# Performance work log

Measured on AMD Instinct MI355X. Metric: run time of the kernel, lower is better.

## Reference

```python
import jax, jax.numpy as jnp
import numpy as np

B, N, F_IN = 16, 2048, 6
NUM_CLASSES = 16


def _laplacian(x):
    # x: [B,N,F]; Gaussian adjacency from pairwise sq distances, then sym-normalized Laplacian
    sq = jnp.sum(x * x, axis=-1, keepdims=True)            # [B,N,1]
    d2 = sq - 2.0 * jnp.einsum('bnf,bmf->bnm', x, x) + jnp.swapaxes(sq, 1, 2)
    adj = jnp.exp(-d2)                                      # [B,N,N]
    dinv = 1.0 / jnp.sqrt(jnp.sum(adj, axis=-1))            # [B,N]
    return jnp.eye(N, dtype=x.dtype) - adj * dinv[:, :, None] * dinv[:, None, :]


def _cheb(x, L, W, b):
    # Chebyshev conv: W [K,Fin,Fout], recursion x_k = 2 L x_{k-1} - x_{k-2}
    K = W.shape[0]
    x0 = x
    out = jnp.einsum('bnf,fg->bng', x0, W[0])
    if K > 1:
        x1 = jnp.einsum('bnm,bmf->bnf', L, x0)
        out = out + jnp.einsum('bnf,fg->bng', x1, W[1])
        for k in range(2, K):
            x2 = 2.0 * jnp.einsum('bnm,bmf->bnf', L, x1) - x0
            out = out + jnp.einsum('bnf,fg->bng', x2, W[k])
            x0, x1 = x1, x2
    return out + b


def setup_inputs() -> dict:
    key = jax.random.key(0)
    ks = jax.random.split(key, 16)

    def w(k, shape, fan_in):
        return jax.random.normal(k, shape, dtype=jnp.float32) * (1.0 / np.sqrt(fan_in))

    inp = {
        'x': jax.random.normal(ks[0], (B, N, F_IN), dtype=jnp.float32),
        'cat': jax.random.randint(ks[1], (B, 1), 0, NUM_CLASSES),
        'W1': w(ks[2], (6, 22, 128), 22), 'b1': jnp.zeros((128,), jnp.float32),
        'W2': w(ks[3], (5, 128, 512), 128), 'b2': jnp.zeros((512,), jnp.float32),
        'W3': w(ks[4], (3, 512, 1024), 512), 'b3': jnp.zeros((1024,), jnp.float32),
        'fc1_w': w(ks[5], (1024, 512), 1024), 'fc1_b': jnp.zeros((512,), jnp.float32),
        'fc2_w': w(ks[6], (1024, 128), 1024), 'fc2_b': jnp.zeros((128,), jnp.float32),
        'fc3_w': w(ks[7], (128, 50), 128), 'fc3_b': jnp.zeros((50,), jnp.float32),
        'br0': jnp.zeros((1, 1, 128), jnp.float32),
        'br1': jnp.zeros((1, 1, 512), jnp.float32),
        'br2': jnp.zeros((1, 1, 1024), jnp.float32),
        'br3': jnp.zeros((1, 1, 512), jnp.float32),
        'br4': jnp.zeros((1, 1, 128), jnp.float32),
        'br5': jnp.zeros((1, 1, 50), jnp.float32),
    }
    return inp


def reference(x, cat, W1, b1, W2, b2, W3, b3, fc1_w, fc1_b, fc2_w, fc2_b,
              fc3_w, fc3_b, br0, br1, br2, br3, br4, br5):
    L = _laplacian(x)                                        # computed under no_grad in torch
    oh = jax.nn.one_hot(cat[:, 0], NUM_CLASSES, dtype=x.dtype)   # [B,16]
    cat_tiled = jnp.broadcast_to(oh[:, None, :], (x.shape[0], N, NUM_CLASSES))
    h = jnp.concatenate([x, cat_tiled], axis=2)              # [B,N,22]

    h = jax.nn.relu(_cheb(h, L, W1, b1) + br0)               # [B,N,128]
    h = jax.nn.relu(_cheb(h, L, W2, b2) + br1)               # [B,N,512]
    x1 = h
    h = jax.nn.relu(_cheb(h, L, W3, b3) + br2)               # [B,N,1024]

    h = jax.nn.relu(h @ fc1_w + fc1_b + br3)                 # [B,N,512]
    h = jnp.concatenate([h, x1], axis=2)                     # [B,N,1024]
    h = jax.nn.relu(h @ fc2_w + fc2_b + br4)                 # [B,N,128]
    h = jax.nn.relu(h @ fc3_w + fc3_b + br5)                 # [B,N,50]
    return h
```

## Files before the change

### kernel.cpp

```cpp
#include <hip/hip_runtime.h>

#define BB 16
#define NN 2048
#define FIN 6
#define MTOT (BB*NN)

typedef unsigned short u16;
typedef __attribute__((ext_vector_type(8))) short  short8;
typedef __attribute__((ext_vector_type(4))) float  f32x4;

__device__ inline float ldf(const u16* p) {
  unsigned u = ((unsigned)*p) << 16; float f; __builtin_memcpy(&f, &u, 4); return f;
}
__device__ inline u16 tobf(float v) {
  unsigned u; __builtin_memcpy(&u, &v, 4);
  u = (u + 0x7FFFu + ((u >> 16) & 1u)) >> 16;
  return (u16)u;
}
__device__ inline void stf(u16* p, float v) { *p = tobf(v); }

__device__ __forceinline__ void gload16(const u16* g, u16* l) {
  __builtin_amdgcn_global_load_lds(
      (const __attribute__((address_space(1))) void*)g,
      (__attribute__((address_space(3))) void*)l, 16, 0, 0);
}

__global__ __launch_bounds__(256) void k_dpart(const float* __restrict__ x,
                                               float* __restrict__ dsum) {
  __shared__ float xs[512][FIN];
  __shared__ float sqs[512];
  const int b = blockIdx.y;
  const int j0 = blockIdx.z * 512;
  const float* xb = x + (size_t)b * NN * FIN;
  for (int l = threadIdx.x; l < 512 * FIN; l += 256) ((float*)xs)[l] = xb[(size_t)j0 * FIN + l];
  __syncthreads();
  for (int j = threadIdx.x; j < 512; j += 256) {
    float s = 0.f;
#pragma unroll
    for (int f = 0; f < FIN; ++f) { float v = xs[j][f]; s = fmaf(v, v, s); }
    sqs[j] = s;
  }
  __syncthreads();
  const int i = blockIdx.x * 256 + threadIdx.x;
  float xi[FIN];
#pragma unroll
  for (int f = 0; f < FIN; ++f) xi[f] = xb[(size_t)i * FIN + f];
  float sqi = 0.f;
#pragma unroll
  for (int f = 0; f < FIN; ++f) sqi = fmaf(xi[f], xi[f], sqi);
  float a0 = 0.f, a1 = 0.f, a2 = 0.f, a3 = 0.f;
  for (int j = 0; j < 512; j += 4) {
#pragma unroll
    for (int u = 0; u < 4; ++u) {
      const int jj = j + u;
      float dot = 0.f;
#pragma unroll
      for (int f = 0; f < FIN; ++f) dot = fmaf(xs[jj][f], xi[f], dot);
      const float e = __expf(2.f * dot - sqi - sqs[jj]);
      if (u == 0) a0 += e; else if (u == 1) a1 += e; else if (u == 2) a2 += e; else a3 += e;
    }
  }
  atomicAdd(&dsum[b * NN + i], (a0 + a1) + (a2 + a3));
}

__global__ void k_rsq(float* __restrict__ d) {
  const int i = blockIdx.x * 256 + threadIdx.x;
  d[i] = 1.0f / sqrtf(d[i]);
}

__global__ __launch_bounds__(256) void k_lap(const float* __restrict__ x,
                                             const float* __restrict__ dinv,
                                             u16* __restrict__ Lm) {
  const int b = blockIdx.z;
  const int i0 = blockIdx.y * 32;
  const int j0 = blockIdx.x * 256;
  __shared__ float xi[32][FIN];
  __shared__ float di[32];
  const int t = threadIdx.x;
  const float* xb = x + (size_t)b * NN * FIN;
  if (t < 32 * FIN) ((float*)xi)[t] = xb[i0 * FIN + t];
  if (t >= 224) di[t - 224] = dinv[b * NN + i0 + (t - 224)];
  const int j = j0 + t;
  float xj[FIN];
#pragma unroll
  for (int f = 0; f < FIN; ++f) xj[f] = xb[j * FIN + f];
  float sqj = 0.f;
#pragma unroll
  for (int f = 0; f < FIN; ++f) sqj = fmaf(xj[f], xj[f], sqj);
  const float dj = dinv[b * NN + j];
  __syncthreads();
  u16* Lb = Lm + (size_t)b * NN * NN;
#pragma unroll 4
  for (int ii = 0; ii < 32; ++ii) {
    float sqi = 0.f, dot = 0.f;
#pragma unroll
    for (int f = 0; f < FIN; ++f) {
      const float v = xi[ii][f];
      sqi = fmaf(v, v, sqi);
      dot = fmaf(v, xj[f], dot);
    }
    float val = -__expf(2.f * dot - sqi - sqj) * di[ii] * dj;
    if (i0 + ii == j) val += 1.f;
    stf(&Lb[(size_t)(i0 + ii) * NN + j], val);
  }
}

__global__ void k_h0T(const float* __restrict__ x, const int* __restrict__ cat,
                      u16* __restrict__ T1T) {
  const int c = blockIdx.y;
  const int m = blockIdx.x * 256 + threadIdx.x;
  float v;
  if (c < 6) v = x[(size_t)m * 6 + c];
  else v = (cat[m >> 11] == (c - 6)) ? 1.f : 0.f;
  stf(&T1T[(size_t)c * MTOT + m], v);
}

__global__ void k_wt(const float* __restrict__ in, u16* __restrict__ out,
                     int R, int C, int ldo) {
  const int r = blockIdx.x * 256 + threadIdx.x;
  const int c = blockIdx.y;
  if (r < R) stf(&out[(size_t)c * ldo + r], in[(size_t)r * C + c]);
}

__global__ __launch_bounds__(256) void k_actT(const u16* __restrict__ in,
                                              u16* __restrict__ out, int F, int ldo) {
  __shared__ u16 t[64][70];
  const int m0 = blockIdx.x * 64;
  const int f0 = blockIdx.y * 64;
  const int tid = threadIdx.x;
#pragma unroll
  for (int v = 0; v < 4; ++v) {
    const int flat = v * 256 + tid;
    const int fr = flat >> 4;
    const int mq = (flat & 15) * 4;
    ushort4 val = {0, 0, 0, 0};
    if (f0 + fr < F) val = *(const ushort4*)&in[(size_t)(f0 + fr) * MTOT + m0 + mq];
    t[fr][mq + 0] = val.x; t[fr][mq + 1] = val.y;
    t[fr][mq + 2] = val.z; t[fr][mq + 3] = val.w;
  }
  __syncthreads();
#pragma unroll
  for (int v = 0; v < 4; ++v) {
    const int flat = v * 256 + tid;
    const int mr = flat >> 4;
    const int fq = (flat & 15) * 4;
    if (f0 + fq >= F) continue;
    u16* dst = &out[(size_t)(m0 + mr) * ldo + f0 + fq];
    if (f0 + fq + 3 < F) {
      ushort4 o;
      o.x = t[fq + 0][mr]; o.y = t[fq + 1][mr];
      o.z = t[fq + 2][mr]; o.w = t[fq + 3][mr];
      *(ushort4*)dst = o;
    } else {
#pragma unroll
      for (int e = 0; e < 4; ++e)
        if (f0 + fq + e < F) dst[e] = t[fq + e][mr];
    }
  }
}

template <int BM, int BN, int EPI, bool TWOQ, typename OT>
__global__ __launch_bounds__(256) void k_mmL(
    const u16* __restrict__ P, long ldp, int rowsP, long strideP,
    const u16* __restrict__ Q0, long ldq0,
    const u16* __restrict__ Q1, long ldq1, int ksplitT,
    int rowsQ, long strideQ, int K,
    OT* __restrict__ Out, long ldo, long strideO,
    const u16* __restrict__ Prev, float alpha, float beta,
    const float* __restrict__ bias, const float* __restrict__ br, int biasOnI) {
  const int b = blockIdx.z;
  const int i0 = blockIdx.y * BM;
  const int j0 = blockIdx.x * BN;
  const u16* Pb = P + (size_t)b * strideP;
  const u16* Qb0 = Q0 + (size_t)b * strideQ;
  OT* Ob = Out + (size_t)b * strideO;
  const u16* Vb = Prev ? Prev + (size_t)b * strideO : nullptr;

  __shared__ __align__(16) u16 Ps[BM * 64];
  __shared__ __align__(16) u16 Qs[BN * 64];
  const int tid = threadIdx.x;
  const int lane = tid & 63;
  const int w = tid >> 6;
  const int wr = w >> 1, wc = w & 1;
  constexpr int FI = BM / 32;
  constexpr int FJ = BN / 32;
  constexpr int VP = BM / 32;
  constexpr int VQ = BN / 32;
  const int rl = lane >> 3;
  const int kb = (((lane & 7) ^ rl) << 3);

  const u16* prow[VP];
  bool pok[VP];
#pragma unroll
  for (int v = 0; v < VP; ++v) {
    const int c = w + v * 4;
    const int gr = i0 + c * 8 + rl;
    pok[v] = gr < rowsP;
    prow[v] = Pb + (size_t)gr * ldp + kb;
  }
  const u16* qrow[VQ];
  const u16* qrow1[TWOQ ? VQ : 1];
  bool qok[VQ];
#pragma unroll
  for (int v = 0; v < VQ; ++v) {
    const int c = w + v * 4;
    const int gr = j0 + c * 8 + rl;
    qok[v] = gr < rowsQ;
    qrow[v] = Qb0 + (size_t)gr * ldq0 + kb;
    if (TWOQ) qrow1[v] = Q1 + (size_t)b * strideQ + (size_t)gr * ldq1 + kb;
  }

  f32x4 acc[FI][FJ];
#pragma unroll
  for (int i = 0; i < FI; ++i)
#pragma unroll
    for (int j = 0; j < FJ; ++j) acc[i][j] = (f32x4){0.f, 0.f, 0.f, 0.f};

  const int nt = K >> 6;
  for (int t = 0; t < nt; ++t) {
#pragma unroll
    for (int v = 0; v < VP; ++v)
      if (pok[v]) gload16(prow[v] + t * 64, &Ps[(w + v * 4) * 512]);
    if (TWOQ) {
      const bool r1 = (t >= ksplitT);
      const int tq = r1 ? (t - ksplitT) : t;
#pragma unroll
      for (int v = 0; v < VQ; ++v)
        if (qok[v]) gload16((r1 ? qrow1[v] : qrow[v]) + tq * 64, &Qs[(w + v * 4) * 512]);
    } else {
#pragma unroll
      for (int v = 0; v < VQ; ++v)
        if (qok[v]) gload16(qrow[v] + t * 64, &Qs[(w + v * 4) * 512]);
    }
    __syncthreads();
#pragma unroll
    for (int h = 0; h < 2; ++h) {
      short8 pf[FI], qf[FJ];
#pragma unroll
      for (int i = 0; i < FI; ++i) {
        const int r = wr * (BM / 2) + i * 16 + (lane & 15);
        const int c = (h * 32 + ((lane >> 4) * 8)) ^ ((r & 7) << 3);
        pf[i] = *(const short8*)&Ps[r * 64 + c];
      }
#pragma unroll
      for (int j = 0; j < FJ; ++j) {
        const int r = wc * (BN / 2) + j * 16 + (lane & 15);
        const int c = (h * 32 + ((lane >> 4) * 8)) ^ ((r & 7) << 3);
        qf[j] = *(const short8*)&Qs[r * 64 + c];
      }
#pragma unroll
      for (int i = 0; i < FI; ++i)
#pragma unroll
        for (int j = 0; j < FJ; ++j)
          acc[i][j] = __builtin_amdgcn_mfma_f32_16x16x32_bf16(pf[i], qf[j], acc[i][j], 0, 0, 0);
    }
    __syncthreads();
  }

  const int ibase = i0 + wr * (BM / 2);
  const int jbase = j0 + wc * (BN / 2);
#pragma unroll
  for (int j = 0; j < FJ; ++j) {
    const int jj = jbase + j * 16 + (lane & 15);
    if (jj >= rowsQ) continue;
    float bj = 0.f;
    if (EPI == 1 && !biasOnI) bj = bias[jj] + br[jj];
#pragma unroll
    for (int i = 0; i < FI; ++i) {
      const int ii = ibase + i * 16 + ((lane >> 4) << 2);
      f32x4 a = acc[i][j];
      float v[4];
#pragma unroll
      for (int e = 0; e < 4; ++e) {
        float xv = a[e];
        if (EPI == 0) {
          xv *= alpha;
          if (beta != 0.f) xv = fmaf(beta, ldf(&Vb[(size_t)jj * ldo + ii + e]), xv);
        } else {
          float bb = bj;
          if (biasOnI) bb = (ii + e < rowsP) ? (bias[ii + e] + br[ii + e]) : 0.f;
          xv = fmaxf(xv + bb, 0.f);
        }
        v[e] = xv;
      }
      if constexpr (sizeof(OT) == 2) {
        u16* dst = (u16*)&Ob[(size_t)jj * ldo + ii];
        if (ii + 3 < rowsP) {
          ushort4 o; o.x = tobf(v[0]); o.y = tobf(v[1]); o.z = tobf(v[2]); o.w = tobf(v[3]);
          *(ushort4*)dst = o;
        } else {
#pragma unroll
          for (int e = 0; e < 4; ++e) if (ii + e < rowsP) dst[e] = tobf(v[e]);
        }
      } else {
        float* dst = (float*)&Ob[(size_t)jj * ldo + ii];
#pragma unroll
        for (int e = 0; e < 4; ++e) if (ii + e < rowsP) dst[e] = v[e];
      }
    }
  }
}

extern "C" void kernel_launch(void* const* d_in, const int* in_sizes, int n_in,
                              void* d_out, int out_size, void* d_ws, size_t ws_size,
                              hipStream_t stream) {
  const float* x    = (const float*)d_in[0];
  const int*   cat  = (const int*)  d_in[1];
  const float* W1   = (const float*)d_in[2];
  const float* b1   = (const float*)d_in[3];
  const float* W2   = (const float*)d_in[4];
  const float* b2   = (const float*)d_in[5];
  const float* W3   = (const float*)d_in[6];
  const float* b3   = (const float*)d_in[7];
  const float* fc1w = (const float*)d_in[8];
  const float* fc1b = (const float*)d_in[9];
  const float* fc2w = (const float*)d_in[10];
  const float* fc2b = (const float*)d_in[11];
  const float* fc3w = (const float*)d_in[12];
  const float* fc3b = (const float*)d_in[13];
  const float* br0  = (const float*)d_in[14];
  const float* br1  = (const float*)d_in[15];
  const float* br2  = (const float*)d_in[16];
  const float* br3  = (const float*)d_in[17];
  const float* br4  = (const float*)d_in[18];
  const float* br5  = (const float*)d_in[19];

  if (ws_size < 240054784ull) return;

  u16* ws = (u16*)d_ws;
  u16* Wt1p = ws;
  u16* Wt2  = Wt1p + 24576;
  u16* Wt3  = Wt2 + 327680;
  u16* Wtf1 = Wt3 + 1572864;
  u16* Wtf2 = Wtf1 + 524288;
  u16* Wtf3 = Wtf2 + 131072;
  u16* Lbuf = ws + 2586880;
  u16* ACT  = Lbuf + 67108864;

  float* dinv = (float*)ACT;
  u16* T1T   = ACT;
  u16* L1rm  = ACT + 4325376;
  u16* T2T   = ACT;
  u16* L2rm  = ACT + 20971520;
  u16* T3T   = ACT;
  u16* L3rm  = Lbuf;
  u16* h3rm  = ACT;
  u16* fc1o  = ACT + 33554432;
  u16* h5    = ACT;

  const long MT = MTOT;
  const int BIG = 1 << 28;

  hipMemsetAsync(dinv, 0, (size_t)MTOT * 4, stream);
  hipMemsetAsync(Wt1p, 0, 24576 * 2, stream);
  hipMemsetAsync(L1rm, 0, (size_t)MTOT * 192 * 2, stream);

  k_wt<<<dim3(1, 128), 256, 0, stream>>>(W1, Wt1p, 132, 128, 192);
  k_wt<<<dim3(3, 512), 256, 0, stream>>>(W2, Wt2, 640, 512, 640);
  k_wt<<<dim3(6, 1024), 256, 0, stream>>>(W3, Wt3, 1536, 1024, 1536);
  k_wt<<<dim3(4, 512), 256, 0, stream>>>(fc1w, Wtf1, 1024, 512, 1024);
  k_wt<<<dim3(4, 128), 256, 0, stream>>>(fc2w, Wtf2, 1024, 128, 1024);
  k_wt<<<dim3(1, 50), 256, 0, stream>>>(fc3w, Wtf3, 128, 50, 128);

  k_dpart<<<dim3(8, BB, 4), 256, 0, stream>>>(x, dinv);
  k_rsq<<<dim3(MTOT / 256), 256, 0, stream>>>(dinv);
  k_lap<<<dim3(8, 64, BB), 256, 0, stream>>>(x, dinv, Lbuf);

  k_h0T<<<dim3(128, 22), 256, 0, stream>>>(x, cat, T1T);
  {
    const size_t s = (size_t)22 * MT;
    k_mmL<64, 32, 0, false, u16><<<dim3(1, 32, BB), 256, 0, stream>>>(
        Lbuf, NN, NN, (long)NN * NN, T1T, MT, nullptr, 0, BIG, 22, NN,
        NN, T1T + s, MT, NN, nullptr, 1.f, 0.f, nullptr, nullptr, 0);
    for (int k = 2; k < 6; ++k)
      k_mmL<64, 32, 0, false, u16><<<dim3(1, 32, BB), 256, 0, stream>>>(
          Lbuf, NN, NN, (long)NN * NN, T1T + (k - 1) * s, MT, nullptr, 0, BIG, 22, NN,
          NN, T1T + k * s, MT, NN, T1T + (k - 2) * s, 2.f, -1.f, nullptr, nullptr, 0);
  }
  k_actT<<<dim3(512, 3), 256, 0, stream>>>(T1T, L1rm, 132, 192);
  k_mmL<128, 128, 1, false, u16><<<dim3(1, 256, 1), 256, 0, stream>>>(
      L1rm, 192, MTOT, 0, Wt1p, 192, nullptr, 0, BIG, 128, 0,
      192, T2T, MT, 0, nullptr, 0.f, 0.f, b1, br0, 0);

  {
    const size_t s = (size_t)128 * MT;
    k_mmL<64, 128, 0, false, u16><<<dim3(1, 32, BB), 256, 0, stream>>>(
        Lbuf, NN, NN, (long)NN * NN, T2T, MT, nullptr, 0, BIG, 128, NN,
        NN, T2T + s, MT, NN, nullptr, 1.f, 0.f, nullptr, nullptr, 0);
    for (int k = 2; k < 5; ++k)
      k_mmL<64, 128, 0, false, u16><<<dim3(1, 32, BB), 256, 0, stream>>>(
          Lbuf, NN, NN, (long)NN * NN, T2T + (k - 1) * s, MT, nullptr, 0, BIG, 128, NN,
          NN, T2T + k * s, MT, NN, T2T + (k - 2) * s, 2.f, -1.f, nullptr, nullptr, 0);
  }
  k_actT<<<dim3(512, 10), 256, 0, stream>>>(T2T, L2rm, 640, 640);
  k_mmL<128, 128, 1, false, u16><<<dim3(4, 256, 1), 256, 0, stream>>>(
      L2rm, 640, MTOT, 0, Wt2, 640, nullptr, 0, BIG, 512, 0,
      640, T3T, MT, 0, nullptr, 0.f, 0.f, b2, br1, 0);

  {
    const size_t s = (size_t)512 * MT;
    k_mmL<128, 128, 0, false, u16><<<dim3(4, 16, BB), 256, 0, stream>>>(
        Lbuf, NN, NN, (long)NN * NN, T3T, MT, nullptr, 0, BIG, 512, NN,
        NN, T3T + s, MT, NN, nullptr, 1.f, 0.f, nullptr, nullptr, 0);
    k_mmL<128, 128, 0, false, u16><<<dim3(4, 16, BB), 256, 0, stream>>>(
        Lbuf, NN, NN, (long)NN * NN, T3T + s, MT, nullptr, 0, BIG, 512, NN,
        NN, T3T + 2 * s, MT, NN, T3T, 2.f, -1.f, nullptr, nullptr, 0);
  }
  k_actT<<<dim3(512, 24), 256, 0, stream>>>(T3T, L3rm, 1536, 1536);
  k_mmL<128, 128, 1, false, u16><<<dim3(256, 8, 1), 256, 0, stream>>>(
      Wt3, 1536, 1024, 0, L3rm, 1536, nullptr, 0, BIG, MTOT, 0,
      1536, h3rm, 1024, 0, nullptr, 0.f, 0.f, b3, br2, 1);

  k_mmL<128, 128, 1, false, u16><<<dim3(256, 4, 1), 256, 0, stream>>>(
      Wtf1, 1024, 512, 0, h3rm, 1024, nullptr, 0, BIG, MTOT, 0,
      1024, fc1o, 512, 0, nullptr, 0.f, 0.f, fc1b, br3, 1);
  k_mmL<64, 128, 1, true, u16><<<dim3(256, 2, 1), 256, 0, stream>>>(
      Wtf2, 1024, 128, 0, fc1o, 512, L3rm, 1536, 8, MTOT, 0,
      1024, h5, 128, 0, nullptr, 0.f, 0.f, fc2b, br4, 1);
  k_mmL<64, 128, 1, false, float><<<dim3(256, 1, 1), 256, 0, stream>>>(
      Wtf3, 128, 50, 0, h5, 128, nullptr, 0, BIG, MTOT, 0,
      128, (float*)d_out, 50, 0, nullptr, 0.f, 0.f, fc3b, br5, 1);
}
```

Measured before the change: 1.125 ms.

## Double-buffer LDS tiles in k_mmL to overlap global loads with MFMA

Doubles the shared-memory P and Q tiles and restructures the K loop so that the next tile's global-to-LDS loads are issued before computing on the current tile. It also replaces the two __syncthreads per iteration with a single vmcnt wait plus barrier. The aim is to hide global load latency behind the MFMA work. In exchange, LDS use doubles, which may reduce occupancy for large BM/BN tiles.

```diff
diff --git a/kernel.cpp b/kernel.cpp
--- a/kernel.cpp
+++ b/kernel.cpp
@@ -176,8 +176,8 @@
   OT* Ob = Out + (size_t)b * strideO;
   const u16* Vb = Prev ? Prev + (size_t)b * strideO : nullptr;
 
-  __shared__ __align__(16) u16 Ps[BM * 64];
-  __shared__ __align__(16) u16 Qs[BN * 64];
+  __shared__ __align__(16) u16 Ps[2][BM * 64];
+  __shared__ __align__(16) u16 Qs[2][BN * 64];
   const int tid = threadIdx.x;
   const int lane = tid & 63;
   const int w = tid >> 6;
@@ -216,23 +216,24 @@
 #pragma unroll
     for (int j = 0; j < FJ; ++j) acc[i][j] = (f32x4){0.f, 0.f, 0.f, 0.f};
 
-  const int nt = K >> 6;
-  for (int t = 0; t < nt; ++t) {
+  auto stage = [&](int t, int buf) {
 #pragma unroll
     for (int v = 0; v < VP; ++v)
-      if (pok[v]) gload16(prow[v] + t * 64, &Ps[(w + v * 4) * 512]);
+      if (pok[v]) gload16(prow[v] + t * 64, &Ps[buf][(w + v * 4) * 512]);
     if (TWOQ) {
       const bool r1 = (t >= ksplitT);
       const int tq = r1 ? (t - ksplitT) : t;
 #pragma unroll
       for (int v = 0; v < VQ; ++v)
-        if (qok[v]) gload16((r1 ? qrow1[v] : qrow[v]) + tq * 64, &Qs[(w + v * 4) * 512]);
+        if (qok[v]) gload16((r1 ? qrow1[v] : qrow[v]) + tq * 64, &Qs[buf][(w + v * 4) * 512]);
     } else {
 #pragma unroll
       for (int v = 0; v < VQ; ++v)
-        if (qok[v]) gload16(qrow[v] + t * 64, &Qs[(w + v * 4) * 512]);
-    }
-    __syncthreads();
+        if (qok[v]) gload16(qrow[v] + t * 64, &Qs[buf][(w + v * 4) * 512]);
+    }
+  };
+
+  auto compute = [&](int buf) {
 #pragma unroll
     for (int h = 0; h < 2; ++h) {
       short8 pf[FI], qf[FJ];
@@ -240,13 +241,13 @@
       for (int i = 0; i < FI; ++i) {
         const int r = wr * (BM / 2) + i * 16 + (lane & 15);
         const int c = (h * 32 + ((lane >> 4) * 8)) ^ ((r & 7) << 3);
-        pf[i] = *(const short8*)&Ps[r * 64 + c];
+        pf[i] = *(const short8*)&Ps[buf][r * 64 + c];
       }
 #pragma unroll
       for (int j = 0; j < FJ; ++j) {
         const int r = wc * (BN / 2) + j * 16 + (lane & 15);
         const int c = (h * 32 + ((lane >> 4) * 8)) ^ ((r & 7) << 3);
-        qf[j] = *(const short8*)&Qs[r * 64 + c];
+        qf[j] = *(const short8*)&Qs[buf][r * 64 + c];
       }
 #pragma unroll
       for (int i = 0; i < FI; ++i)
@@ -254,7 +255,20 @@
         for (int j = 0; j < FJ; ++j)
           acc[i][j] = __builtin_amdgcn_mfma_f32_16x16x32_bf16(pf[i], qf[j], acc[i][j], 0, 0, 0);
     }
-    __syncthreads();
+  };
+
+  const int nt = K >> 6;
+  stage(0, 0);
+  asm volatile("s_waitcnt vmcnt(0)" ::: "memory");
+  __builtin_amdgcn_s_barrier();
+  __builtin_amdgcn_sched_barrier(0);
+  for (int t = 0; t < nt; ++t) {
+    const int cur = t & 1;
+    if (t + 1 < nt) stage(t + 1, cur ^ 1);
+    compute(cur);
+    asm volatile("s_waitcnt vmcnt(0)" ::: "memory");
+    __builtin_amdgcn_s_barrier();
+    __builtin_amdgcn_sched_barrier(0);
   }
 
   const int ibase = i0 + wr * (BM / 2);
```

Result: no change. 1.141 ms (+1.4%).

## Swizzle GEMM workgroups across XCDs, fuse rsqrt into Laplacian, drop padding memset

Applied to the files above, without the earlier changes.

Adds a template-selected block-index remap to the GEMM kernel so consecutive workgroup IDs are spread across the 8 XCDs, aiming to improve L2 locality on shared operand tiles. Folds the 1/sqrt degree normalisation into the Laplacian builder, which now handles four columns per thread with 8-byte vectorised stores. The transpose kernel now writes zero padding columns itself, removing a large memset. The remap adds integer index arithmetic per block and may hurt locality for some grid shapes.

```diff
diff --git a/kernel.cpp b/kernel.cpp
--- a/kernel.cpp
+++ b/kernel.cpp
@@ -63,45 +63,50 @@
   atomicAdd(&dsum[b * NN + i], (a0 + a1) + (a2 + a3));
 }
 
-__global__ void k_rsq(float* __restrict__ d) {
-  const int i = blockIdx.x * 256 + threadIdx.x;
-  d[i] = 1.0f / sqrtf(d[i]);
-}
-
 __global__ __launch_bounds__(256) void k_lap(const float* __restrict__ x,
-                                             const float* __restrict__ dinv,
+                                             const float* __restrict__ dsum,
                                              u16* __restrict__ Lm) {
   const int b = blockIdx.z;
   const int i0 = blockIdx.y * 32;
-  const int j0 = blockIdx.x * 256;
+  const int j0 = blockIdx.x * 1024;
   __shared__ float xi[32][FIN];
   __shared__ float di[32];
   const int t = threadIdx.x;
   const float* xb = x + (size_t)b * NN * FIN;
   if (t < 32 * FIN) ((float*)xi)[t] = xb[i0 * FIN + t];
-  if (t >= 224) di[t - 224] = dinv[b * NN + i0 + (t - 224)];
-  const int j = j0 + t;
-  float xj[FIN];
-#pragma unroll
-  for (int f = 0; f < FIN; ++f) xj[f] = xb[j * FIN + f];
-  float sqj = 0.f;
-#pragma unroll
-  for (int f = 0; f < FIN; ++f) sqj = fmaf(xj[f], xj[f], sqj);
-  const float dj = dinv[b * NN + j];
+  if (t >= 224) di[t - 224] = 1.0f / sqrtf(dsum[b * NN + i0 + (t - 224)]);
+  const int j = j0 + t * 4;
+  float xj[4][FIN], sqj[4], dj[4];
+#pragma unroll
+  for (int u = 0; u < 4; ++u) {
+    float s = 0.f;
+#pragma unroll
+    for (int f = 0; f < FIN; ++f) {
+      const float v = xb[(size_t)(j + u) * FIN + f];
+      xj[u][f] = v; s = fmaf(v, v, s);
+    }
+    sqj[u] = s;
+    dj[u] = 1.0f / sqrtf(dsum[b * NN + j + u]);
+  }
   __syncthreads();
   u16* Lb = Lm + (size_t)b * NN * NN;
-#pragma unroll 4
+#pragma unroll 2
   for (int ii = 0; ii < 32; ++ii) {
-    float sqi = 0.f, dot = 0.f;
-#pragma unroll
-    for (int f = 0; f < FIN; ++f) {
-      const float v = xi[ii][f];
-      sqi = fmaf(v, v, sqi);
-      dot = fmaf(v, xj[f], dot);
-    }
-    float val = -__expf(2.f * dot - sqi - sqj) * di[ii] * dj;
-    if (i0 + ii == j) val += 1.f;
-    stf(&Lb[(size_t)(i0 + ii) * NN + j], val);
+    float sqi = 0.f;
+#pragma unroll
+    for (int f = 0; f < FIN; ++f) { const float v = xi[ii][f]; sqi = fmaf(v, v, sqi); }
+    u16 o[4];
+#pragma unroll
+    for (int u = 0; u < 4; ++u) {
+      float dot = 0.f;
+#pragma unroll
+      for (int f = 0; f < FIN; ++f) dot = fmaf(xi[ii][f], xj[u][f], dot);
+      float val = -__expf(2.f * dot - sqi - sqj[u]) * di[ii] * dj[u];
+      if (i0 + ii == j + u) val += 1.f;
+      o[u] = tobf(val);
+    }
+    ushort4 ov; ov.x = o[0]; ov.y = o[1]; ov.z = o[2]; ov.w = o[3];
+    *(ushort4*)&Lb[(size_t)(i0 + ii) * NN + j] = ov;
   }
 }
 
@@ -123,7 +128,8 @@
 }
 
 __global__ __launch_bounds__(256) void k_actT(const u16* __restrict__ in,
-                                              u16* __restrict__ out, int F, int ldo) {
+                                              u16* __restrict__ out, int F,
+                                              int ldo, int Fw) {
   __shared__ u16 t[64][70];
   const int m0 = blockIdx.x * 64;
   const int f0 = blockIdx.y * 64;
@@ -144,9 +150,9 @@
     const int flat = v * 256 + tid;
     const int mr = flat >> 4;
     const int fq = (flat & 15) * 4;
-    if (f0 + fq >= F) continue;
+    if (f0 + fq >= Fw) continue;
     u16* dst = &out[(size_t)(m0 + mr) * ldo + f0 + fq];
-    if (f0 + fq + 3 < F) {
+    if (f0 + fq + 3 < Fw) {
       ushort4 o;
       o.x = t[fq + 0][mr]; o.y = t[fq + 1][mr];
       o.z = t[fq + 2][mr]; o.w = t[fq + 3][mr];
@@ -154,12 +160,12 @@
     } else {
 #pragma unroll
       for (int e = 0; e < 4; ++e)
-        if (f0 + fq + e < F) dst[e] = t[fq + e][mr];
-    }
-  }
-}
-
-template <int BM, int BN, int EPI, bool TWOQ, typename OT>
+        if (f0 + fq + e < Fw) dst[e] = t[fq + e][mr];
+    }
+  }
+}
+
+template <int BM, int BN, int EPI, bool TWOQ, int SWZ, typename OT>
 __global__ __launch_bounds__(256) void k_mmL(
     const u16* __restrict__ P, long ldp, int rowsP, long strideP,
     const u16* __restrict__ Q0, long ldq0,
@@ -168,9 +174,18 @@
     OT* __restrict__ Out, long ldo, long strideO,
     const u16* __restrict__ Prev, float alpha, float beta,
     const float* __restrict__ bias, const float* __restrict__ br, int biasOnI) {
-  const int b = blockIdx.z;
-  const int i0 = blockIdx.y * BM;
-  const int j0 = blockIdx.x * BN;
+  int bx = blockIdx.x, by = blockIdx.y, bz = blockIdx.z;
+  if (SWZ != 0) {
+    const int gx = gridDim.x, gy = gridDim.y;
+    const int nwg = gx * gy * gridDim.z;
+    const int o = bx + gx * (by + gy * bz);
+    const int Lg = (o & 7) * (nwg >> 3) + (o >> 3);
+    if (SWZ == 1) { bx = Lg % gx; by = (Lg / gx) % gy; bz = Lg / (gx * gy); }
+    else          { by = Lg % gy; bx = (Lg / gy) % gx; bz = Lg / (gx * gy); }
+  }
+  const int b = bz;
+  const int i0 = by * BM;
+  const int j0 = bx * BN;
   const u16* Pb = P + (size_t)b * strideP;
   const u16* Qb0 = Q0 + (size_t)b * strideQ;
   OT* Ob = Out + (size_t)b * strideO;
@@ -337,7 +352,7 @@
   u16* Lbuf = ws + 2586880;
   u16* ACT  = Lbuf + 67108864;
 
-  float* dinv = (float*)ACT;
+  float* dsum = (float*)ACT;
   u16* T1T   = ACT;
   u16* L1rm  = ACT + 4325376;
   u16* T2T   = ACT;
@@ -351,9 +366,8 @@
   const long MT = MTOT;
   const int BIG = 1 << 28;
 
-  hipMemsetAsync(dinv, 0, (size_t)MTOT * 4, stream);
+  hipMemsetAsync(dsum, 0, (size_t)MTOT * 4, stream);
   hipMemsetAsync(Wt1p, 0, 24576 * 2, stream);
-  hipMemsetAsync(L1rm, 0, (size_t)MTOT * 192 * 2, stream);
 
   k_wt<<<dim3(1, 128), 256, 0, stream>>>(W1, Wt1p, 132, 128, 192);
   k_wt<<<dim3(3, 512), 256, 0, stream>>>(W2, Wt2, 640, 512, 640);
@@ -362,62 +376,61 @@
   k_wt<<<dim3(4, 128), 256, 0, stream>>>(fc2w, Wtf2, 1024, 128, 1024);
   k_wt<<<dim3(1, 50), 256, 0, stream>>>(fc3w, Wtf3, 128, 50, 128);
 
-  k_dpart<<<dim3(8, BB, 4), 256, 0, stream>>>(x, dinv);
-  k_rsq<<<dim3(MTOT / 256), 256, 0, stream>>>(dinv);
-  k_lap<<<dim3(8, 64, BB), 256, 0, stream>>>(x, dinv, Lbuf);
+  k_dpart<<<dim3(8, BB, 4), 256, 0, stream>>>(x, dsum);
+  k_lap<<<dim3(2, 64, BB), 256, 0, stream>>>(x, dsum, Lbuf);
 
   k_h0T<<<dim3(128, 22), 256, 0, stream>>>(x, cat, T1T);
   {
     const size_t s = (size_t)22 * MT;
-    k_mmL<64, 32, 0, false, u16><<<dim3(1, 32, BB), 256, 0, stream>>>(
+    k_mmL<64, 32, 0, false, 1, u16><<<dim3(1, 32, BB), 256, 0, stream>>>(
         Lbuf, NN, NN, (long)NN * NN, T1T, MT, nullptr, 0, BIG, 22, NN,
         NN, T1T + s, MT, NN, nullptr, 1.f, 0.f, nullptr, nullptr, 0);
     for (int k = 2; k < 6; ++k)
-      k_mmL<64, 32, 0, false, u16><<<dim3(1, 32, BB), 256, 0, stream>>>(
+      k_mmL<64, 32, 0, false, 1, u16><<<dim3(1, 32, BB), 256, 0, stream>>>(
           Lbuf, NN, NN, (long)NN * NN, T1T + (k - 1) * s, MT, nullptr, 0, BIG, 22, NN,
           NN, T1T + k * s, MT, NN, T1T + (k - 2) * s, 2.f, -1.f, nullptr, nullptr, 0);
   }
-  k_actT<<<dim3(512, 3), 256, 0, stream>>>(T1T, L1rm, 132, 192);
-  k_mmL<128, 128, 1, false, u16><<<dim3(1, 256, 1), 256, 0, stream>>>(
+  k_actT<<<dim3(512, 3), 256, 0, stream>>>(T1T, L1rm, 132, 192, 192);
+  k_mmL<128, 128, 1, false, 2, u16><<<dim3(1, 256, 1), 256, 0, stream>>>(
       L1rm, 192, MTOT, 0, Wt1p, 192, nullptr, 0, BIG, 128, 0,
       192, T2T, MT, 0, nullptr, 0.f, 0.f, b1, br0, 0);
 
   {
     const size_t s = (size_t)128 * MT;
-    k_mmL<64, 128, 0, false, u16><<<dim3(1, 32, BB), 256, 0, stream>>>(
+    k_mmL<64, 128, 0, false, 1, u16><<<dim3(1, 32, BB), 256, 0, stream>>>(
         Lbuf, NN, NN, (long)NN * NN, T2T, MT, nullptr, 0, BIG, 128, NN,
         NN, T2T + s, MT, NN, nullptr, 1.f, 0.f, nullptr, nullptr, 0);
     for (int k = 2; k < 5; ++k)
-      k_mmL<64, 128, 0, false, u16><<<dim3(1, 32, BB), 256, 0, stream>>>(
+      k_mmL<64, 128, 0, false, 1, u16><<<dim3(1, 32, BB), 256, 0, stream>>>(
           Lbuf, NN, NN, (long)NN * NN, T2T + (k - 1) * s, MT, nullptr, 0, BIG, 128, NN,
           NN, T2T + k * s, MT, NN, T2T + (k - 2) * s, 2.f, -1.f, nullptr, nullptr, 0);
   }
-  k_actT<<<dim3(512, 10), 256, 0, stream>>>(T2T, L2rm, 640, 640);
-  k_mmL<128, 128, 1, false, u16><<<dim3(4, 256, 1), 256, 0, stream>>>(
+  k_actT<<<dim3(512, 10), 256, 0, stream>>>(T2T, L2rm, 640, 640, 640);
+  k_mmL<128, 128, 1, false, 2, u16><<<dim3(4, 256, 1), 256, 0, stream>>>(
       L2rm, 640, MTOT, 0, Wt2, 640, nullptr, 0, BIG, 512, 0,
       640, T3T, MT, 0, nullptr, 0.f, 0.f, b2, br1, 0);
 
   {
     const size_t s = (size_t)512 * MT;
-    k_mmL<128, 128, 0, false, u16><<<dim3(4, 16, BB), 256, 0, stream>>>(
+    k_mmL<128, 128, 0, false, 1, u16><<<dim3(4, 16, BB), 256, 0, stream>>>(
         Lbuf, NN, NN, (long)NN * NN, T3T, MT, nullptr, 0, BIG, 512, NN,
         NN, T3T + s, MT, NN, nullptr, 1.f, 0.f, nullptr, nullptr, 0);
-    k_mmL<128, 128, 0, false, u16><<<dim3(4, 16, BB), 256, 0, stream>>>(
+    k_mmL<128, 128, 0, false, 1, u16><<<dim3(4, 16, BB), 256, 0, stream>>>(
         Lbuf, NN, NN, (long)NN * NN, T3T + s, MT, nullptr, 0, BIG, 512, NN,
         NN, T3T + 2 * s, MT, NN, T3T, 2.f, -1.f, nullptr, nullptr, 0);
   }
-  k_actT<<<dim3(512, 24), 256, 0, stream>>>(T3T, L3rm, 1536, 1536);
-  k_mmL<128, 128, 1, false, u16><<<dim3(256, 8, 1), 256, 0, stream>>>(
+  k_actT<<<dim3(512, 24), 256, 0, stream>>>(T3T, L3rm, 1536, 1536, 1536);
+  k_mmL<128, 128, 1, false, 2, u16><<<dim3(256, 8, 1), 256, 0, stream>>>(
       Wt3, 1536, 1024, 0, L3rm, 1536, nullptr, 0, BIG, MTOT, 0,
       1536, h3rm, 1024, 0, nullptr, 0.f, 0.f, b3, br2, 1);
 
-  k_mmL<128, 128, 1, false, u16><<<dim3(256, 4, 1), 256, 0, stream>>>(
+  k_mmL<128, 128, 1, false, 2, u16><<<dim3(256, 4, 1), 256, 0, stream>>>(
       Wtf1, 1024, 512, 0, h3rm, 1024, nullptr, 0, BIG, MTOT, 0,
       1024, fc1o, 512, 0, nullptr, 0.f, 0.f, fc1b, br3, 1);
-  k_mmL<64, 128, 1, true, u16><<<dim3(256, 2, 1), 256, 0, stream>>>(
+  k_mmL<64, 128, 1, true, 2, u16><<<dim3(256, 2, 1), 256, 0, stream>>>(
       Wtf2, 1024, 128, 0, fc1o, 512, L3rm, 1536, 8, MTOT, 0,
       1024, h5, 128, 0, nullptr, 0.f, 0.f, fc2b, br4, 1);
-  k_mmL<64, 128, 1, false, float><<<dim3(256, 1, 1), 256, 0, stream>>>(
+  k_mmL<64, 128, 1, false, 2, float><<<dim3(256, 1, 1), 256, 0, stream>>>(
       Wtf3, 128, 50, 0, h5, 128, nullptr, 0, BIG, MTOT, 0,
       128, (float*)d_out, 50, 0, nullptr, 0.f, 0.f, fc3b, br5, 1);
 }
```

After: 1.095 ms. -2.7%, faster.
